# Kernel optimization log

Hardware: AMD Instinct MI355X
Metric: run time of the kernel (lower is better)

The kernel has to match this reference:

```python
import jax, jax.numpy as jnp
import numpy as np

N = 500_000   # total nodes
D = 256       # in_dim
G = 1024      # num graphs (segments)
H = max(32, D // 2)  # gate hidden = 128
L = D // 2    # local pool dim = 128


def setup_inputs() -> dict:
    key = jax.random.key(0)
    ks = jax.random.split(key, 8)
    x = jax.random.normal(ks[0], (N, D), dtype=jnp.float32)
    batch = jnp.sort(jax.random.randint(ks[1], (N,), 0, G, dtype=jnp.int32))
    s = 0.02
    w1 = jax.random.normal(ks[2], (D, H), dtype=jnp.float32) * s
    b1 = jnp.zeros((H,), dtype=jnp.float32)
    w2 = jax.random.normal(ks[3], (H, 1), dtype=jnp.float32) * s
    b2 = jnp.zeros((1,), dtype=jnp.float32)
    lp_w = jax.random.normal(ks[4], (D, L), dtype=jnp.float32) * s
    lp_b = jnp.zeros((L,), dtype=jnp.float32)
    return {"x": x, "batch": batch, "w1": w1, "b1": b1, "w2": w2,
            "b2": b2, "lp_w": lp_w, "lp_b": lp_b}


def reference(x, batch, w1, b1, w2, b2, lp_w, lp_b):
    # segment counts (guard empty segments)
    ones = jnp.ones((x.shape[0],), dtype=x.dtype)
    cnt = jax.ops.segment_sum(ones, batch, num_segments=G)
    cnt = jnp.maximum(cnt, 1.0)[:, None]                      # [G,1]

    # mean pool
    mean_p = jax.ops.segment_sum(x, batch, num_segments=G) / cnt

    # max pool
    max_p = jax.ops.segment_max(x, batch, num_segments=G)

    # global attention pool: gate MLP -> per-segment softmax -> weighted sum
    # (Dropout is identity at inference.)
    h = jax.nn.gelu(x @ w1 + b1, approximate=False)           # [N,H]
    gate = (h @ w2 + b2)[:, 0]                                # [N]
    gmax = jax.ops.segment_max(gate, batch, num_segments=G)   # [G]
    e = jnp.exp(gate - gmax[batch])                           # [N]
    denom = jax.ops.segment_sum(e, batch, num_segments=G)     # [G]
    a = e / denom[batch]                                      # [N] softmax per graph
    att_p = jax.ops.segment_sum(a[:, None] * x, batch, num_segments=G)

    # local MLP pool then mean
    local = jax.nn.gelu(x @ lp_w + lp_b, approximate=False)   # [N,L]
    local_mean = jax.ops.segment_sum(local, batch, num_segments=G) / cnt

    return jnp.concatenate([mean_p, max_p, att_p, local_mean], axis=-1)  # [G, 3D + D//2]
```

## Files before the change

kernel.cpp:

```cpp
#include <hip/hip_runtime.h>
#include <hip/hip_bf16.h>
#include <float.h>
#include <math.h>


typedef __bf16 bf16;
typedef __bf16 bf16x4 __attribute__((ext_vector_type(4)));
typedef __bf16 bf16x8 __attribute__((ext_vector_type(8)));
typedef float f32x4 __attribute__((ext_vector_type(4)));

#define D 256
#define HDIM 128
#define LDIM 128

__device__ __forceinline__ float gelu_f(float v) {
    return 0.5f * v * (1.0f + erff(v * 0.70710678118654752f));
}

__global__ __launch_bounds__(256) void k_prep(const float* __restrict__ w1,
                                              const float* __restrict__ lpw,
                                              bf16* __restrict__ w1T,
                                              bf16* __restrict__ lpT,
                                              float* __restrict__ local_sum,
                                              int* __restrict__ segstart,
                                              int G, int N) {
    int t = blockIdx.x * 256 + threadIdx.x;
    if (t == 0) segstart[G] = N;
    if (t < G * LDIM) local_sum[t] = 0.0f;
    if (t < HDIM * D) {
        int n = t >> 8;
        int k = t & 255;
        w1T[t] = (bf16)w1[k * HDIM + n];
        lpT[t] = (bf16)lpw[k * LDIM + n];
    }
}

__global__ __launch_bounds__(256, 3) void k_gate_local(
    const float* __restrict__ x, const int* __restrict__ batch,
    const bf16* __restrict__ w1T, const float* __restrict__ b1,
    const float* __restrict__ w2, const float* __restrict__ b2,
    const bf16* __restrict__ lpT, const float* __restrict__ lpb,
    float* __restrict__ gate, float* __restrict__ local_sum, int N)
{
    __shared__ bf16 xs[64][264];
    __shared__ int bs[64];
    __shared__ float gpart[4][64];

    const int tid  = threadIdx.x;
    const int wave = tid >> 6;
    const int lane = tid & 63;
    const int quad = lane >> 4;
    const int l16  = lane & 15;
    const long base = (long)blockIdx.x * 64;

    #pragma unroll
    for (int it = 0; it < 16; ++it) {
        int idx = it * 256 + tid;
        int row = idx >> 6;
        int c4  = idx & 63;
        long node = base + row;
        float4 v;
        if (node < N) v = *(const float4*)(x + node * D + c4 * 4);
        else          v = make_float4(0.f, 0.f, 0.f, 0.f);
        bf16x4 pk;
        pk[0] = (bf16)v.x; pk[1] = (bf16)v.y; pk[2] = (bf16)v.z; pk[3] = (bf16)v.w;
        *(bf16x4*)(&xs[row][c4 * 4]) = pk;
    }
    if (tid < 64) bs[tid] = (base + tid < N) ? batch[base + tid] : 0x7fffffff;
    __syncthreads();

    const int c0 = wave * 32 + l16;
    const int c1 = c0 + 16;

    f32x4 zero = {0.f, 0.f, 0.f, 0.f};
    f32x4 h0[4], h1[4], l0[4], l1[4];
    #pragma unroll
    for (int mt = 0; mt < 4; ++mt) { h0[mt] = zero; h1[mt] = zero; l0[mt] = zero; l1[mt] = zero; }

    #pragma unroll
    for (int kt = 0; kt < 8; ++kt) {
        int k0 = kt * 32 + quad * 8;
        bf16x8 bw0 = *(const bf16x8*)(w1T + c0 * D + k0);
        bf16x8 bw1 = *(const bf16x8*)(w1T + c1 * D + k0);
        bf16x8 bp0 = *(const bf16x8*)(lpT + c0 * D + k0);
        bf16x8 bp1 = *(const bf16x8*)(lpT + c1 * D + k0);
        #pragma unroll
        for (int mt = 0; mt < 4; ++mt) {
            bf16x8 a = *(const bf16x8*)(&xs[mt * 16 + l16][k0]);
            h0[mt] = __builtin_amdgcn_mfma_f32_16x16x32_bf16(a, bw0, h0[mt], 0, 0, 0);
            h1[mt] = __builtin_amdgcn_mfma_f32_16x16x32_bf16(a, bw1, h1[mt], 0, 0, 0);
            l0[mt] = __builtin_amdgcn_mfma_f32_16x16x32_bf16(a, bp0, l0[mt], 0, 0, 0);
            l1[mt] = __builtin_amdgcn_mfma_f32_16x16x32_bf16(a, bp1, l1[mt], 0, 0, 0);
        }
    }

    {
        const float b1c0 = b1[c0], b1c1 = b1[c1];
        const float w2c0 = w2[c0], w2c1 = w2[c1];
        #pragma unroll
        for (int mt = 0; mt < 4; ++mt) {
            #pragma unroll
            for (int r = 0; r < 4; ++r) {
                float v = gelu_f(h0[mt][r] + b1c0) * w2c0
                        + gelu_f(h1[mt][r] + b1c1) * w2c1;
                v += __shfl_down(v, 8, 16);
                v += __shfl_down(v, 4, 16);
                v += __shfl_down(v, 2, 16);
                v += __shfl_down(v, 1, 16);
                if (l16 == 0) gpart[wave][mt * 16 + quad * 4 + r] = v;
            }
        }
    }
    __syncthreads();
    if (tid < 64) {
        long node = base + tid;
        if (node < N)
            gate[node] = gpart[0][tid] + gpart[1][tid] + gpart[2][tid] + gpart[3][tid] + b2[0];
    }

    const float lb0 = lpb[c0], lb1 = lpb[c1];
    const bool fast = (base + 63 < N) && (bs[0] == bs[63]);
    if (fast) {
        float s0 = 0.f, s1 = 0.f;
        #pragma unroll
        for (int mt = 0; mt < 4; ++mt) {
            #pragma unroll
            for (int r = 0; r < 4; ++r) {
                s0 += gelu_f(l0[mt][r] + lb0);
                s1 += gelu_f(l1[mt][r] + lb1);
            }
        }
        s0 += __shfl_xor(s0, 16); s0 += __shfl_xor(s0, 32);
        s1 += __shfl_xor(s1, 16); s1 += __shfl_xor(s1, 32);
        if (quad == 0) {
            int g = bs[0];
            atomicAdd(&local_sum[g * LDIM + c0], s0);
            atomicAdd(&local_sum[g * LDIM + c1], s1);
        }
    } else {
        int cur = -1;
        float s0 = 0.f, s1 = 0.f;
        #pragma unroll
        for (int mt = 0; mt < 4; ++mt) {
            #pragma unroll
            for (int r = 0; r < 4; ++r) {
                int lrow = mt * 16 + quad * 4 + r;
                if (base + lrow < N) {
                    int g = bs[lrow];
                    if (g != cur) {
                        if (cur >= 0) {
                            atomicAdd(&local_sum[cur * LDIM + c0], s0);
                            atomicAdd(&local_sum[cur * LDIM + c1], s1);
                        }
                        cur = g; s0 = 0.f; s1 = 0.f;
                    }
                    s0 += gelu_f(l0[mt][r] + lb0);
                    s1 += gelu_f(l1[mt][r] + lb1);
                }
            }
        }
        if (cur >= 0) {
            atomicAdd(&local_sum[cur * LDIM + c0], s0);
            atomicAdd(&local_sum[cur * LDIM + c1], s1);
        }
    }
}

__device__ __forceinline__ int lower_bound_i(const int* a, int n, int v) {
    int lo = 0, hi = n;
    while (lo < hi) { int mid = (lo + hi) >> 1; if (a[mid] < v) lo = mid + 1; else hi = mid; }
    return lo;
}

__global__ __launch_bounds__(256) void k_stats(
    const int* __restrict__ batch, const float* __restrict__ gate,
    float* __restrict__ aw, float* __restrict__ segdenom,
    int* __restrict__ segstart, int N)
{
    const int g   = blockIdx.x;
    const int tid = threadIdx.x;
    const int wave = tid >> 6;
    const int lane = tid & 63;

    __shared__ int sse[2];
    __shared__ float wred[4];

    if (tid == 0) sse[0] = lower_bound_i(batch, N, g);
    if (tid == 1) sse[1] = lower_bound_i(batch, N, g + 1);
    __syncthreads();
    const int start = sse[0], end = sse[1];
    if (tid == 0) segstart[g] = start;

    float m = -FLT_MAX;
    for (int i = start + tid; i < end; i += 256) m = fmaxf(m, gate[i]);
    #pragma unroll
    for (int off = 32; off > 0; off >>= 1) m = fmaxf(m, __shfl_xor(m, off));
    if (lane == 0) wred[wave] = m;
    __syncthreads();
    m = fmaxf(fmaxf(wred[0], wred[1]), fmaxf(wred[2], wred[3]));
    __syncthreads();

    float s = 0.f;
    for (int i = start + tid; i < end; i += 256) {
        float e = expf(gate[i] - m);
        aw[i] = e;
        s += e;
    }
    #pragma unroll
    for (int off = 32; off > 0; off >>= 1) s += __shfl_xor(s, off);
    if (lane == 0) wred[wave] = s;
    __syncthreads();
    if (tid == 0) segdenom[g] = wred[0] + wred[1] + wred[2] + wred[3];
}

__global__ __launch_bounds__(256) void k_pool(
    const float* __restrict__ x,
    const float* __restrict__ aw, const float* __restrict__ segdenom,
    const int* __restrict__ segstart, const float* __restrict__ local_sum,
    float* __restrict__ out)
{
    const int g    = blockIdx.x >> 1;
    const int half = blockIdx.x & 1;
    const int tid  = threadIdx.x;
    const int rg   = tid >> 5;
    const int c4   = tid & 31;

    __shared__ float psum[8][128];
    __shared__ float pmax[8][128];
    __shared__ float patt[8][128];

    const int start = segstart[g];
    const int end   = segstart[g + 1];
    const int cnt   = end - start;

    const float* xb = x + half * 128 + c4 * 4;

    float sx = 0, sy = 0, sz = 0, sw = 0;
    float ax = 0, ay = 0, az = 0, aw4 = 0;
    float mx = -FLT_MAX, my = -FLT_MAX, mz = -FLT_MAX, mw = -FLT_MAX;

    int i = start + rg;
    #define POOL_BODY(ri)                                                    \
        {                                                                    \
            float e = aw[ri];                                                \
            float4 v = *(const float4*)(xb + (long)(ri) * D);                \
            sx += v.x; sy += v.y; sz += v.z; sw += v.w;                      \
            ax += e * v.x; ay += e * v.y; az += e * v.z; aw4 += e * v.w;     \
            mx = fmaxf(mx, v.x); my = fmaxf(my, v.y);                        \
            mz = fmaxf(mz, v.z); mw = fmaxf(mw, v.w);                        \
        }
    for (; i + 8 < end; i += 16) { POOL_BODY(i); POOL_BODY(i + 8); }
    if (i < end) POOL_BODY(i);
    #undef POOL_BODY

    const int cb = c4 * 4;
    psum[rg][cb] = sx; psum[rg][cb+1] = sy; psum[rg][cb+2] = sz; psum[rg][cb+3] = sw;
    patt[rg][cb] = ax; patt[rg][cb+1] = ay; patt[rg][cb+2] = az; patt[rg][cb+3] = aw4;
    pmax[rg][cb] = mx; pmax[rg][cb+1] = my; pmax[rg][cb+2] = mz; pmax[rg][cb+3] = mw;
    __syncthreads();

    const float inv  = 1.0f / fmaxf((float)cnt, 1.0f);
    const float dn   = segdenom[g];
    const float invd = (dn > 0.f) ? 1.0f / dn : 0.f;
    const long  o    = (long)g * 896;

    if (tid < 128) {
        int c = tid;
        float s = 0.f, a = 0.f, mm = -FLT_MAX;
        #pragma unroll
        for (int r = 0; r < 8; ++r) {
            s += psum[r][c];
            a += patt[r][c];
            mm = fmaxf(mm, pmax[r][c]);
        }
        if (cnt == 0) mm = -INFINITY;
        out[o + half * 128 + c]       = s * inv;
        out[o + 256 + half * 128 + c] = mm;
        out[o + 512 + half * 128 + c] = a * invd;
        if (half == 1) out[o + 768 + c] = local_sum[g * LDIM + c] * inv;
    }
}

extern "C" void kernel_launch(void* const* d_in, const int* in_sizes, int n_in,
                              void* d_out, int out_size, void* d_ws, size_t ws_size,
                              hipStream_t stream) {
    const float* x   = (const float*)d_in[0];
    const int* batch = (const int*)d_in[1];
    const float* w1  = (const float*)d_in[2];
    const float* b1  = (const float*)d_in[3];
    const float* w2  = (const float*)d_in[4];
    const float* b2  = (const float*)d_in[5];
    const float* lpw = (const float*)d_in[6];
    const float* lpb = (const float*)d_in[7];
    float* out = (float*)d_out;

    const int N = in_sizes[0] / D;
    const int G = out_size / 896;

    char* ws = (char*)d_ws;
    size_t off = 0;
    float* gate      = (float*)(ws + off); off += (((size_t)N * 4) + 255) & ~(size_t)255;
    float* aw        = (float*)(ws + off); off += (((size_t)N * 4) + 255) & ~(size_t)255;
    bf16*  w1T       = (bf16*)(ws + off);  off += (size_t)HDIM * D * 2;
    bf16*  lpT       = (bf16*)(ws + off);  off += (size_t)LDIM * D * 2;
    float* local_sum = (float*)(ws + off); off += (size_t)G * LDIM * 4;
    float* segdenom  = (float*)(ws + off); off += (size_t)G * 4;
    int*   segstart  = (int*)(ws + off);   off += (size_t)(G + 1) * 4;

    const int prep_threads = G * LDIM;
    k_prep<<<(prep_threads + 255) / 256, 256, 0, stream>>>(w1, lpw, w1T, lpT, local_sum,
                                                           segstart, G, N);
    k_gate_local<<<(int)((N + 63) / 64), 256, 0, stream>>>(x, batch, w1T, b1, w2, b2,
                                                           lpT, lpb, gate, local_sum, N);
    k_stats<<<G, 256, 0, stream>>>(batch, gate, aw, segdenom, segstart, N);
    k_pool<<<2 * G, 256, 0, stream>>>(x, aw, segdenom, segstart, local_sum, out);
}
```

Before: 883.2 us.

## Fuse mean, max and attention pooling into the gate kernel in one pass

```diff
diff --git a/kernel.cpp b/kernel.cpp
--- a/kernel.cpp
+++ b/kernel.cpp
@@ -16,17 +16,23 @@
 __device__ __forceinline__ float gelu_f(float v) {
     return 0.5f * v * (1.0f + erff(v * 0.70710678118654752f));
 }
+__device__ __forceinline__ unsigned fkey(float v) {
+    unsigned u = __float_as_uint(v);
+    return (u & 0x80000000u) ? ~u : (u | 0x80000000u);
+}
+__device__ __forceinline__ float funkey(unsigned k) {
+    unsigned u = (k & 0x80000000u) ? (k ^ 0x80000000u) : ~k;
+    return __uint_as_float(u);
+}
 
 __global__ __launch_bounds__(256) void k_prep(const float* __restrict__ w1,
                                               const float* __restrict__ lpw,
                                               bf16* __restrict__ w1T,
                                               bf16* __restrict__ lpT,
-                                              float* __restrict__ local_sum,
-                                              int* __restrict__ segstart,
-                                              int G, int N) {
+                                              float* __restrict__ zb,
+                                              int ztot) {
     int t = blockIdx.x * 256 + threadIdx.x;
-    if (t == 0) segstart[G] = N;
-    if (t < G * LDIM) local_sum[t] = 0.0f;
+    if (t < ztot) zb[t] = 0.0f;
     if (t < HDIM * D) {
         int n = t >> 8;
         int k = t & 255;
@@ -35,48 +41,98 @@
     }
 }
 
-__global__ __launch_bounds__(256, 3) void k_gate_local(
+__global__ __launch_bounds__(256, 3) void k_main(
     const float* __restrict__ x, const int* __restrict__ batch,
     const bf16* __restrict__ w1T, const float* __restrict__ b1,
     const float* __restrict__ w2, const float* __restrict__ b2,
     const bf16* __restrict__ lpT, const float* __restrict__ lpb,
-    float* __restrict__ gate, float* __restrict__ local_sum, int N)
+    float* __restrict__ meansum, float* __restrict__ attsum,
+    unsigned* __restrict__ maxkey, float* __restrict__ local_sum,
+    float* __restrict__ denom, int N)
 {
     __shared__ bf16 xs[64][264];
+    __shared__ float earr[64];
+    __shared__ float gpart[4][64];
     __shared__ int bs[64];
-    __shared__ float gpart[4][64];
 
     const int tid  = threadIdx.x;
     const int wave = tid >> 6;
     const int lane = tid & 63;
     const int quad = lane >> 4;
     const int l16  = lane & 15;
+    const int rg   = tid >> 6;
+    const int c4   = tid & 63;
     const long base = (long)blockIdx.x * 64;
 
-    #pragma unroll
-    for (int it = 0; it < 16; ++it) {
-        int idx = it * 256 + tid;
-        int row = idx >> 6;
-        int c4  = idx & 63;
-        long node = base + row;
-        float4 v;
-        if (node < N) v = *(const float4*)(x + node * D + c4 * 4);
-        else          v = make_float4(0.f, 0.f, 0.f, 0.f);
-        bf16x4 pk;
-        pk[0] = (bf16)v.x; pk[1] = (bf16)v.y; pk[2] = (bf16)v.z; pk[3] = (bf16)v.w;
-        *(bf16x4*)(&xs[row][c4 * 4]) = pk;
-    }
+    const int g0 = batch[base];
+    const bool fast = (base + 63 < N) && (batch[base + 63] == g0);
+
     if (tid < 64) bs[tid] = (base + tid < N) ? batch[base + tid] : 0x7fffffff;
+
+    float sacc[4] = {0.f, 0.f, 0.f, 0.f};
+    float macc[4] = {-FLT_MAX, -FLT_MAX, -FLT_MAX, -FLT_MAX};
+    if (fast) {
+        #pragma unroll
+        for (int it = 0; it < 16; ++it) {
+            int row = rg + it * 4;
+            float4 v = *(const float4*)(x + (base + row) * (long)D + c4 * 4);
+            bf16x4 pk;
+            pk[0] = (bf16)v.x; pk[1] = (bf16)v.y; pk[2] = (bf16)v.z; pk[3] = (bf16)v.w;
+            *(bf16x4*)(&xs[row][c4 * 4]) = pk;
+            sacc[0] += v.x; sacc[1] += v.y; sacc[2] += v.z; sacc[3] += v.w;
+            macc[0] = fmaxf(macc[0], v.x); macc[1] = fmaxf(macc[1], v.y);
+            macc[2] = fmaxf(macc[2], v.z); macc[3] = fmaxf(macc[3], v.w);
+        }
+    } else {
+        int rung = -1;
+        #pragma unroll
+        for (int it = 0; it < 16; ++it) {
+            int row = rg + it * 4;
+            long node = base + row;
+            float4 v = make_float4(0.f, 0.f, 0.f, 0.f);
+            if (node < N) v = *(const float4*)(x + node * (long)D + c4 * 4);
+            bf16x4 pk;
+            pk[0] = (bf16)v.x; pk[1] = (bf16)v.y; pk[2] = (bf16)v.z; pk[3] = (bf16)v.w;
+            *(bf16x4*)(&xs[row][c4 * 4]) = pk;
+            if (node < N) {
+                int gg = batch[node];
+                if (gg != rung) {
+                    if (rung >= 0) {
+                        float* mp = meansum + (long)rung * 256 + c4 * 4;
+                        unsigned* kp = maxkey + (long)rung * 256 + c4 * 4;
+                        #pragma unroll
+                        for (int j = 0; j < 4; ++j) {
+                            atomicAdd(mp + j, sacc[j]);
+                            atomicMax(kp + j, fkey(macc[j]));
+                        }
+                    }
+                    rung = gg;
+                    sacc[0] = sacc[1] = sacc[2] = sacc[3] = 0.f;
+                    macc[0] = macc[1] = macc[2] = macc[3] = -FLT_MAX;
+                }
+                sacc[0] += v.x; sacc[1] += v.y; sacc[2] += v.z; sacc[3] += v.w;
+                macc[0] = fmaxf(macc[0], v.x); macc[1] = fmaxf(macc[1], v.y);
+                macc[2] = fmaxf(macc[2], v.z); macc[3] = fmaxf(macc[3], v.w);
+            }
+        }
+        if (rung >= 0) {
+            float* mp = meansum + (long)rung * 256 + c4 * 4;
+            unsigned* kp = maxkey + (long)rung * 256 + c4 * 4;
+            #pragma unroll
+            for (int j = 0; j < 4; ++j) {
+                atomicAdd(mp + j, sacc[j]);
+                atomicMax(kp + j, fkey(macc[j]));
+            }
+        }
+    }
     __syncthreads();
 
     const int c0 = wave * 32 + l16;
     const int c1 = c0 + 16;
-
     f32x4 zero = {0.f, 0.f, 0.f, 0.f};
     f32x4 h0[4], h1[4], l0[4], l1[4];
     #pragma unroll
     for (int mt = 0; mt < 4; ++mt) { h0[mt] = zero; h1[mt] = zero; l0[mt] = zero; l1[mt] = zero; }
-
     #pragma unroll
     for (int kt = 0; kt < 8; ++kt) {
         int k0 = kt * 32 + quad * 8;
@@ -114,55 +170,124 @@
     __syncthreads();
     if (tid < 64) {
         long node = base + tid;
-        if (node < N)
-            gate[node] = gpart[0][tid] + gpart[1][tid] + gpart[2][tid] + gpart[3][tid] + b2[0];
-    }
-
-    const float lb0 = lpb[c0], lb1 = lpb[c1];
-    const bool fast = (base + 63 < N) && (bs[0] == bs[63]);
-    if (fast) {
-        float s0 = 0.f, s1 = 0.f;
-        #pragma unroll
-        for (int mt = 0; mt < 4; ++mt) {
-            #pragma unroll
-            for (int r = 0; r < 4; ++r) {
-                s0 += gelu_f(l0[mt][r] + lb0);
-                s1 += gelu_f(l1[mt][r] + lb1);
-            }
-        }
-        s0 += __shfl_xor(s0, 16); s0 += __shfl_xor(s0, 32);
-        s1 += __shfl_xor(s1, 16); s1 += __shfl_xor(s1, 32);
-        if (quad == 0) {
-            int g = bs[0];
-            atomicAdd(&local_sum[g * LDIM + c0], s0);
-            atomicAdd(&local_sum[g * LDIM + c1], s1);
-        }
-    } else {
-        int cur = -1;
-        float s0 = 0.f, s1 = 0.f;
-        #pragma unroll
-        for (int mt = 0; mt < 4; ++mt) {
-            #pragma unroll
-            for (int r = 0; r < 4; ++r) {
-                int lrow = mt * 16 + quad * 4 + r;
-                if (base + lrow < N) {
-                    int g = bs[lrow];
-                    if (g != cur) {
-                        if (cur >= 0) {
-                            atomicAdd(&local_sum[cur * LDIM + c0], s0);
-                            atomicAdd(&local_sum[cur * LDIM + c1], s1);
-                        }
-                        cur = g; s0 = 0.f; s1 = 0.f;
-                    }
+        float gv = gpart[0][tid] + gpart[1][tid] + gpart[2][tid] + gpart[3][tid] + b2[0];
+        float e = (node < N) ? expf(gv) : 0.f;
+        earr[tid] = e;
+        if (fast) {
+            float t = e;
+            t += __shfl_xor(t, 1);  t += __shfl_xor(t, 2);  t += __shfl_xor(t, 4);
+            t += __shfl_xor(t, 8);  t += __shfl_xor(t, 16); t += __shfl_xor(t, 32);
+            if (tid == 0) atomicAdd(&denom[g0], t);
+        } else if (node < N) {
+            atomicAdd(&denom[bs[tid]], e);
+        }
+    }
+    __syncthreads();
+
+    {
+        const float lb0 = lpb[c0], lb1 = lpb[c1];
+        if (fast) {
+            float s0 = 0.f, s1 = 0.f;
+            #pragma unroll
+            for (int mt = 0; mt < 4; ++mt) {
+                #pragma unroll
+                for (int r = 0; r < 4; ++r) {
                     s0 += gelu_f(l0[mt][r] + lb0);
                     s1 += gelu_f(l1[mt][r] + lb1);
                 }
             }
-        }
-        if (cur >= 0) {
-            atomicAdd(&local_sum[cur * LDIM + c0], s0);
-            atomicAdd(&local_sum[cur * LDIM + c1], s1);
-        }
+            s0 += __shfl_xor(s0, 16); s0 += __shfl_xor(s0, 32);
+            s1 += __shfl_xor(s1, 16); s1 += __shfl_xor(s1, 32);
+            if (quad == 0) {
+                atomicAdd(&local_sum[(long)g0 * LDIM + c0], s0);
+                atomicAdd(&local_sum[(long)g0 * LDIM + c1], s1);
+            }
+        } else {
+            int cur = -1;
+            float s0 = 0.f, s1 = 0.f;
+            #pragma unroll
+            for (int mt = 0; mt < 4; ++mt) {
+                #pragma unroll
+                for (int r = 0; r < 4; ++r) {
+                    int lrow = mt * 16 + quad * 4 + r;
+                    if (base + lrow < N) {
+                        int gg = bs[lrow];
+                        if (gg != cur) {
+                            if (cur >= 0) {
+                                atomicAdd(&local_sum[(long)cur * LDIM + c0], s0);
+                                atomicAdd(&local_sum[(long)cur * LDIM + c1], s1);
+                            }
+                            cur = gg; s0 = 0.f; s1 = 0.f;
+                        }
+                        s0 += gelu_f(l0[mt][r] + lb0);
+                        s1 += gelu_f(l1[mt][r] + lb1);
+                    }
+                }
+            }
+            if (cur >= 0) {
+                atomicAdd(&local_sum[(long)cur * LDIM + c0], s0);
+                atomicAdd(&local_sum[(long)cur * LDIM + c1], s1);
+            }
+        }
+    }
+
+    float aacc[4] = {0.f, 0.f, 0.f, 0.f};
+    if (fast) {
+        #pragma unroll
+        for (int it = 0; it < 16; ++it) {
+            int row = rg + it * 4;
+            float e = earr[row];
+            bf16x4 pv = *(const bf16x4*)(&xs[row][c4 * 4]);
+            aacc[0] += e * (float)pv[0]; aacc[1] += e * (float)pv[1];
+            aacc[2] += e * (float)pv[2]; aacc[3] += e * (float)pv[3];
+        }
+    } else {
+        int rung = -1;
+        #pragma unroll
+        for (int it = 0; it < 16; ++it) {
+            int row = rg + it * 4;
+            if (base + row >= N) break;
+            int gg = bs[row];
+            if (gg != rung) {
+                if (rung >= 0) {
+                    float* ap = attsum + (long)rung * 256 + c4 * 4;
+                    #pragma unroll
+                    for (int j = 0; j < 4; ++j) atomicAdd(ap + j, aacc[j]);
+                }
+                rung = gg;
+                aacc[0] = aacc[1] = aacc[2] = aacc[3] = 0.f;
+            }
+            float e = earr[row];
+            bf16x4 pv = *(const bf16x4*)(&xs[row][c4 * 4]);
+            aacc[0] += e * (float)pv[0]; aacc[1] += e * (float)pv[1];
+            aacc[2] += e * (float)pv[2]; aacc[3] += e * (float)pv[3];
+        }
+        if (rung >= 0) {
+            float* ap = attsum + (long)rung * 256 + c4 * 4;
+            #pragma unroll
+            for (int j = 0; j < 4; ++j) atomicAdd(ap + j, aacc[j]);
+        }
+    }
+    __syncthreads();
+
+    if (fast) {
+        float* xsf = (float*)&xs[0][0];
+        #pragma unroll
+        for (int j = 0; j < 4; ++j) {
+            int c = c4 * 4 + j;
+            xsf[rg * 256 + c]        = sacc[j];
+            xsf[1024 + rg * 256 + c] = macc[j];
+            xsf[2048 + rg * 256 + c] = aacc[j];
+        }
+        __syncthreads();
+        int c = tid;
+        float s = xsf[c] + xsf[256 + c] + xsf[512 + c] + xsf[768 + c];
+        float m = fmaxf(fmaxf(xsf[1024 + c], xsf[1280 + c]),
+                        fmaxf(xsf[1536 + c], xsf[1792 + c]));
+        float a = xsf[2048 + c] + xsf[2304 + c] + xsf[2560 + c] + xsf[2816 + c];
+        atomicAdd(&meansum[(long)g0 * 256 + c], s);
+        atomicMax(&maxkey[(long)g0 * 256 + c], fkey(m));
+        atomicAdd(&attsum[(long)g0 * 256 + c], a);
     }
 }
 
@@ -172,113 +297,28 @@
     return lo;
 }
 
-__global__ __launch_bounds__(256) void k_stats(
-    const int* __restrict__ batch, const float* __restrict__ gate,
-    float* __restrict__ aw, float* __restrict__ segdenom,
-    int* __restrict__ segstart, int N)
+__global__ __launch_bounds__(256) void k_final(
+    const int* __restrict__ batch,
+    const float* __restrict__ meansum, const float* __restrict__ attsum,
+    const unsigned* __restrict__ maxkey, const float* __restrict__ local_sum,
+    const float* __restrict__ denom, float* __restrict__ out, int N)
 {
     const int g   = blockIdx.x;
     const int tid = threadIdx.x;
-    const int wave = tid >> 6;
-    const int lane = tid & 63;
-
     __shared__ int sse[2];
-    __shared__ float wred[4];
-
     if (tid == 0) sse[0] = lower_bound_i(batch, N, g);
     if (tid == 1) sse[1] = lower_bound_i(batch, N, g + 1);
     __syncthreads();
-    const int start = sse[0], end = sse[1];
-    if (tid == 0) segstart[g] = start;
-
-    float m = -FLT_MAX;
-    for (int i = start + tid; i < end; i += 256) m = fmaxf(m, gate[i]);
-    #pragma unroll
-    for (int off = 32; off > 0; off >>= 1) m = fmaxf(m, __shfl_xor(m, off));
-    if (lane == 0) wred[wave] = m;
-    __syncthreads();
-    m = fmaxf(fmaxf(wred[0], wred[1]), fmaxf(wred[2], wred[3]));
-    __syncthreads();
-
-    float s = 0.f;
-    for (int i = start + tid; i < end; i += 256) {
-        float e = expf(gate[i] - m);
-        aw[i] = e;
-        s += e;
-    }
-    #pragma unroll
-    for (int off = 32; off > 0; off >>= 1) s += __shfl_xor(s, off);
-    if (lane == 0) wred[wave] = s;
-    __syncthreads();
-    if (tid == 0) segdenom[g] = wred[0] + wred[1] + wred[2] + wred[3];
-}
-
-__global__ __launch_bounds__(256) void k_pool(
-    const float* __restrict__ x,
-    const float* __restrict__ aw, const float* __restrict__ segdenom,
-    const int* __restrict__ segstart, const float* __restrict__ local_sum,
-    float* __restrict__ out)
-{
-    const int g    = blockIdx.x >> 1;
-    const int half = blockIdx.x & 1;
-    const int tid  = threadIdx.x;
-    const int rg   = tid >> 5;
-    const int c4   = tid & 31;
-
-    __shared__ float psum[8][128];
-    __shared__ float pmax[8][128];
-    __shared__ float patt[8][128];
-
-    const int start = segstart[g];
-    const int end   = segstart[g + 1];
-    const int cnt   = end - start;
-
-    const float* xb = x + half * 128 + c4 * 4;
-
-    float sx = 0, sy = 0, sz = 0, sw = 0;
-    float ax = 0, ay = 0, az = 0, aw4 = 0;
-    float mx = -FLT_MAX, my = -FLT_MAX, mz = -FLT_MAX, mw = -FLT_MAX;
-
-    int i = start + rg;
-    #define POOL_BODY(ri)                                                    \
-        {                                                                    \
-            float e = aw[ri];                                                \
-            float4 v = *(const float4*)(xb + (long)(ri) * D);                \
-            sx += v.x; sy += v.y; sz += v.z; sw += v.w;                      \
-            ax += e * v.x; ay += e * v.y; az += e * v.z; aw4 += e * v.w;     \
-            mx = fmaxf(mx, v.x); my = fmaxf(my, v.y);                        \
-            mz = fmaxf(mz, v.z); mw = fmaxf(mw, v.w);                        \
-        }
-    for (; i + 8 < end; i += 16) { POOL_BODY(i); POOL_BODY(i + 8); }
-    if (i < end) POOL_BODY(i);
-    #undef POOL_BODY
-
-    const int cb = c4 * 4;
-    psum[rg][cb] = sx; psum[rg][cb+1] = sy; psum[rg][cb+2] = sz; psum[rg][cb+3] = sw;
-    patt[rg][cb] = ax; patt[rg][cb+1] = ay; patt[rg][cb+2] = az; patt[rg][cb+3] = aw4;
-    pmax[rg][cb] = mx; pmax[rg][cb+1] = my; pmax[rg][cb+2] = mz; pmax[rg][cb+3] = mw;
-    __syncthreads();
-
-    const float inv  = 1.0f / fmaxf((float)cnt, 1.0f);
-    const float dn   = segdenom[g];
+    const int cnt = sse[1] - sse[0];
+    const float inv = 1.0f / fmaxf((float)cnt, 1.0f);
+    const float dn  = denom[g];
     const float invd = (dn > 0.f) ? 1.0f / dn : 0.f;
-    const long  o    = (long)g * 896;
-
-    if (tid < 128) {
-        int c = tid;
-        float s = 0.f, a = 0.f, mm = -FLT_MAX;
-        #pragma unroll
-        for (int r = 0; r < 8; ++r) {
-            s += psum[r][c];
-            a += patt[r][c];
-            mm = fmaxf(mm, pmax[r][c]);
-        }
-        if (cnt == 0) mm = -INFINITY;
-        out[o + half * 128 + c]       = s * inv;
-        out[o + 256 + half * 128 + c] = mm;
-        out[o + 512 + half * 128 + c] = a * invd;
-        if (half == 1) out[o + 768 + c] = local_sum[g * LDIM + c] * inv;
-    }
+    const long o = (long)g * 896;
+
+    out[o + tid]       = meansum[(long)g * 256 + tid] * inv;
+    out[o + 256 + tid] = (cnt == 0) ? -INFINITY : funkey(maxkey[(long)g * 256 + tid]);
+    out[o + 512 + tid] = attsum[(long)g * 256 + tid] * invd;
+    if (tid < 128) out[o + 768 + tid] = local_sum[(long)g * LDIM + tid] * inv;
 }
 
 extern "C" void kernel_launch(void* const* d_in, const int* in_sizes, int n_in,
@@ -299,19 +339,20 @@
 
     char* ws = (char*)d_ws;
     size_t off = 0;
-    float* gate      = (float*)(ws + off); off += (((size_t)N * 4) + 255) & ~(size_t)255;
-    float* aw        = (float*)(ws + off); off += (((size_t)N * 4) + 255) & ~(size_t)255;
-    bf16*  w1T       = (bf16*)(ws + off);  off += (size_t)HDIM * D * 2;
-    bf16*  lpT       = (bf16*)(ws + off);  off += (size_t)LDIM * D * 2;
-    float* local_sum = (float*)(ws + off); off += (size_t)G * LDIM * 4;
-    float* segdenom  = (float*)(ws + off); off += (size_t)G * 4;
-    int*   segstart  = (int*)(ws + off);   off += (size_t)(G + 1) * 4;
-
-    const int prep_threads = G * LDIM;
-    k_prep<<<(prep_threads + 255) / 256, 256, 0, stream>>>(w1, lpw, w1T, lpT, local_sum,
-                                                           segstart, G, N);
-    k_gate_local<<<(int)((N + 63) / 64), 256, 0, stream>>>(x, batch, w1T, b1, w2, b2,
-                                                           lpT, lpb, gate, local_sum, N);
-    k_stats<<<G, 256, 0, stream>>>(batch, gate, aw, segdenom, segstart, N);
-    k_pool<<<2 * G, 256, 0, stream>>>(x, aw, segdenom, segstart, local_sum, out);
-}
+    const int ztot = G * (256 + 256 + 256 + 128 + 1);
+    float* zb = (float*)(ws + off); off += (((size_t)ztot * 4) + 255) & ~(size_t)255;
+    bf16* w1T = (bf16*)(ws + off);  off += (size_t)HDIM * D * 2;
+    bf16* lpT = (bf16*)(ws + off);  off += (size_t)LDIM * D * 2;
+
+    float*    meansum   = zb;
+    float*    attsum    = zb + (size_t)G * 256;
+    unsigned* maxkey    = (unsigned*)(zb + (size_t)2 * G * 256);
+    float*    local_sum = zb + (size_t)3 * G * 256;
+    float*    denom     = zb + (size_t)3 * G * 256 + (size_t)G * 128;
+
+    k_prep<<<(ztot + 255) / 256, 256, 0, stream>>>(w1, lpw, w1T, lpT, zb, ztot);
+    k_main<<<(int)((N + 63) / 64), 256, 0, stream>>>(x, batch, w1T, b1, w2, b2, lpT, lpb,
+                                                     meansum, attsum, maxkey, local_sum,
+                                                     denom, N);
+    k_final<<<G, 256, 0, stream>>>(batch, meansum, attsum, maxkey, local_sum, denom, out, N);
+}
```

New measurement: 890.6 us. Within noise of the previous version (+0.8%).
